# Optimization experiments

Measured on AMD Instinct MI355X. Metric: run time of the kernel, lower is better.

Reference implementation:

```python
import jax, jax.numpy as jnp
import numpy as np

R_SAFE = 0.8

def setup_inputs() -> dict:
    key = jax.random.key(0)
    ks = jax.random.split(key, 12)
    B, F, H1, H21, H22, C = 524288, 10, 128, 32, 32, 2
    def lin(k, fan_in, fan_out):
        k1, k2 = jax.random.split(k)
        bound = 1.0 / np.sqrt(fan_in)
        W = jax.random.uniform(k1, (fan_out, fan_in), jnp.float32, -bound, bound)
        b = jax.random.uniform(k2, (fan_out,), jnp.float32, -bound, bound)
        return W, b
    W1, b1 = lin(ks[0], F, H1)
    W21, b21 = lin(ks[1], H1, H21)
    W22, b22 = lin(ks[2], H1, H22)
    W31, b31 = lin(ks[3], H21, C)
    W32, b32 = lin(ks[4], H22, 1)
    obs = jax.random.normal(ks[5], (B, F), jnp.float32)
    return {"obs": obs, "W1": W1, "b1": b1, "W21": W21, "b21": b21,
            "W22": W22, "b22": b22, "W31": W31, "b31": b31, "W32": W32, "b32": b32}

def _forward(obs, W1, b1, W21, b21, W22, b22, W31, b31, W32, b32):
    x = jax.nn.silu(obs @ W1.T + b1)          # [B, H1]
    x21 = jax.nn.silu(x @ W21.T + b21)        # [B, H21]
    x22 = jax.nn.silu(x @ W22.T + b22)        # [B, H22]
    unom = x21 @ W31.T + b31                  # [B, 2]
    alpha = 4.0 * jax.nn.sigmoid((x22 @ W32.T + b32)[:, 0])  # [B]
    rel_x, rel_y = obs[:, 6], obs[:, 7]
    v_hx, v_hy = obs[:, 8], obs[:, 9]
    barrier = rel_x**2 + rel_y**2 - R_SAFE**2
    lf = -2.0 * (rel_x * v_hx + rel_y * v_hy)
    # single inequality G u <= h with G = [-2 rel_x, -2 rel_y]
    G = jnp.stack([-2.0 * rel_x, -2.0 * rel_y], axis=1)      # [B, 2]
    h = lf + alpha * barrier                                  # [B]
    # QP: min ||u - unom||^2 s.t. G u <= h  ->  halfspace projection (exact KKT)
    gg = jnp.sum(G * G, axis=1)                               # [B]
    viol = jnp.sum(G * unom, axis=1) - h                      # [B]
    lam = jnp.where(gg > 0, jax.nn.relu(viol) / jnp.maximum(gg, 1e-12), 0.0)
    return unom - lam[:, None] * G

def reference(obs, W1, b1, W21, b21, W22, b22, W31, b31, W32, b32):
    return _forward(obs, W1, b1, W21, b21, W22, b22, W31, b31, W32, b32)
```

## Files before the change

### kernel.cpp

```cpp
#include <hip/hip_runtime.h>


typedef _Float16 half8 __attribute__((ext_vector_type(8)));
typedef float floatx4 __attribute__((ext_vector_type(4)));

#define TPB 256
#define NW  4

#define WS_FRAG 0
#define WS_B2Q  26624

__device__ __forceinline__ float fast_sigmoid(float z) {
    return __builtin_amdgcn_rcpf(1.0f + __expf(-z));
}

__global__ __launch_bounds__(256) void prep_kernel(
    const float* __restrict__ W1,  const float* __restrict__ b1,
    const float* __restrict__ W21, const float* __restrict__ b21,
    const float* __restrict__ W22, const float* __restrict__ b22,
    const float* __restrict__ W31, const float* __restrict__ b31,
    const float* __restrict__ W32, const float* __restrict__ b32,
    unsigned char* __restrict__ ws)
{
    const int tid  = blockIdx.x * 256 + threadIdx.x;
    const int lane = tid & 63;
    const int m    = lane & 15;
    const int q    = lane >> 4;

    if (tid < 26 * 64) {
        const int f = tid >> 6;
        float v[8];
        if (f < 8) {
            const float* wr = W1 + (f * 16 + m) * 10;
            #pragma unroll
            for (int j = 0; j < 8; ++j) {
                const int k = q * 8 + j;
                v[j] = (k < 10) ? wr[k] : (k == 10 ? b1[f * 16 + m] : 0.0f);
            }
        } else if (f < 24) {
            const int f2 = f - 8, nt2 = f2 >> 2, kt = f2 & 3;
            const int n2 = nt2 * 16 + m;
            const float* wr = (n2 < 32) ? (W21 + n2 * 128)
                                        : (W22 + (n2 - 32) * 128);
            #pragma unroll
            for (int j = 0; j < 8; ++j) {
                const int H = (2 * kt + (j >> 2)) * 16 + q * 4 + (j & 3);
                v[j] = wr[H];
            }
        } else {
            const int kt3 = f - 24;
            #pragma unroll
            for (int j = 0; j < 8; ++j) {
                const int H3 = (2 * kt3 + (j >> 2)) * 16 + q * 4 + (j & 3);
                float x = 0.0f;
                if (m == 0)      x = (H3 < 32)  ? W31[H3]       : 0.0f;
                else if (m == 1) x = (H3 < 32)  ? W31[32 + H3]  : 0.0f;
                else if (m == 2) x = (H3 >= 32) ? W32[H3 - 32]  : 0.0f;
                v[j] = x;
            }
        }
        half8 h;
        #pragma unroll
        for (int j = 0; j < 8; ++j) h[j] = (_Float16)v[j];
        ((half8*)(ws + WS_FRAG))[tid] = h;
    }
    if (tid < 16) {
        const int nt2 = tid >> 2, qq = tid & 3;
        float4 v;
        float* vp = (float*)&v;
        #pragma unroll
        for (int r = 0; r < 4; ++r) {
            const int n2 = nt2 * 16 + qq * 4 + r;
            vp[r] = (n2 < 32) ? b21[n2] : b22[n2 - 32];
        }
        ((float4*)(ws + WS_B2Q))[tid] = v;
    }
}

__global__ __launch_bounds__(TPB, 2) void barriernet_kernel(
    const float* __restrict__ obs,
    const unsigned char* __restrict__ ws,
    const float* __restrict__ b31, const float* __restrict__ b32,
    float* __restrict__ out, int B)
{
    const int tid  = threadIdx.x;
    const int wave = tid >> 6;
    const int lane = tid & 63;
    const int m    = lane & 15;
    const int q    = lane >> 4;

    const half8* wf = (const half8*)(ws + WS_FRAG);
    half8 w1f[8], w2f[16], w3f0, w3f1;
    #pragma unroll
    for (int nt = 0; nt < 8; ++nt)  w1f[nt] = wf[nt * 64 + lane];
    #pragma unroll
    for (int f2 = 0; f2 < 16; ++f2) w2f[f2] = wf[(8 + f2) * 64 + lane];
    w3f0 = wf[24 * 64 + lane];
    w3f1 = wf[25 * 64 + lane];

    const float4* bt = (const float4*)(ws + WS_B2Q);
    float4 b2q[4];
    #pragma unroll
    for (int nt2 = 0; nt2 < 4; ++nt2) b2q[nt2] = bt[nt2 * 4 + q];

    const float bu0 = b31[0], bu1 = b31[1], bz3 = b32[0];

    const int tiles = (B + 15) >> 4;
    const int tbase = (blockIdx.x * NW + wave) * 2;

    const float* orow[2];
    half8 xf[2];
    int lrow0[2];
    #pragma unroll
    for (int p = 0; p < 2; ++p) {
        int tile = tbase + p;
        if (tile >= tiles) tile = tiles - 1;
        int lr = (tile << 4) + m;
        if (lr >= B) lr = B - 1;
        lrow0[p] = lr;
        orow[p] = obs + (size_t)lr * 10;

        float g0=0,g1=0,g2=0,g3=0,g4=0,g5=0,g6=0,g7=0;
        if (q == 0) {
            float2 p0 = *(const float2*)(orow[p] + 0);
            float2 p1 = *(const float2*)(orow[p] + 2);
            float2 p2 = *(const float2*)(orow[p] + 4);
            float2 p3 = *(const float2*)(orow[p] + 6);
            g0=p0.x; g1=p0.y; g2=p1.x; g3=p1.y;
            g4=p2.x; g5=p2.y; g6=p3.x; g7=p3.y;
        } else if (q == 1) {
            float2 pp = *(const float2*)(orow[p] + 8);
            g0=pp.x; g1=pp.y;
            g2=1.0f;
        }
        xf[p][0]=(_Float16)g0; xf[p][1]=(_Float16)g1;
        xf[p][2]=(_Float16)g2; xf[p][3]=(_Float16)g3;
        xf[p][4]=(_Float16)g4; xf[p][5]=(_Float16)g5;
        xf[p][6]=(_Float16)g6; xf[p][7]=(_Float16)g7;
    }

    floatx4 acc[2][8];
    #pragma unroll
    for (int nt = 0; nt < 8; ++nt) {
        #pragma unroll
        for (int p = 0; p < 2; ++p) {
            floatx4 z = {0.0f, 0.0f, 0.0f, 0.0f};
            acc[p][nt] = __builtin_amdgcn_mfma_f32_16x16x32_f16(
                             w1f[nt], xf[p], z, 0, 0, 0);
        }
    }

    half8 b2f[2][4];
    #pragma unroll
    for (int p = 0; p < 2; ++p) {
        #pragma unroll
        for (int kt = 0; kt < 4; ++kt) {
            half8 bf;
            #pragma unroll
            for (int jj = 0; jj < 4; ++jj) {
                float z0 = acc[p][2 * kt][jj];
                float z1 = acc[p][2 * kt + 1][jj];
                bf[jj]     = (_Float16)(z0 * fast_sigmoid(z0));
                bf[jj + 4] = (_Float16)(z1 * fast_sigmoid(z1));
            }
            b2f[p][kt] = bf;
        }
    }

    floatx4 acc2[2][4];
    #pragma unroll
    for (int nt2 = 0; nt2 < 4; ++nt2) {
        #pragma unroll
        for (int p = 0; p < 2; ++p) {
            floatx4 z = {b2q[nt2].x, b2q[nt2].y, b2q[nt2].z, b2q[nt2].w};
            #pragma unroll
            for (int kt = 0; kt < 4; ++kt)
                z = __builtin_amdgcn_mfma_f32_16x16x32_f16(
                        w2f[nt2 * 4 + kt], b2f[p][kt], z, 0, 0, 0);
            acc2[p][nt2] = z;
        }
    }

    half8 b3f[2][2];
    #pragma unroll
    for (int p = 0; p < 2; ++p) {
        #pragma unroll
        for (int kt3 = 0; kt3 < 2; ++kt3) {
            half8 bf;
            #pragma unroll
            for (int jj = 0; jj < 4; ++jj) {
                float z0 = acc2[p][2 * kt3][jj];
                float z1 = acc2[p][2 * kt3 + 1][jj];
                bf[jj]     = (_Float16)(z0 * fast_sigmoid(z0));
                bf[jj + 4] = (_Float16)(z1 * fast_sigmoid(z1));
            }
            b3f[p][kt3] = bf;
        }
    }

    #pragma unroll
    for (int p = 0; p < 2; ++p) {
        floatx4 d = {0.0f, 0.0f, 0.0f, 0.0f};
        d = __builtin_amdgcn_mfma_f32_16x16x32_f16(w3f0, b3f[p][0], d, 0, 0, 0);
        d = __builtin_amdgcn_mfma_f32_16x16x32_f16(w3f1, b3f[p][1], d, 0, 0, 0);
        if (q == 0) {
            const float u0  = d[0] + bu0;
            const float u1  = d[1] + bu1;
            const float z32 = d[2] + bz3;
            const float alpha = 4.0f * fast_sigmoid(z32);

            const float2 rxy = *(const float2*)(orow[p] + 6);
            const float2 vxy = *(const float2*)(orow[p] + 8);
            const float rx = rxy.x, ry = rxy.y, vx = vxy.x, vy = vxy.y;

            const float barrier = rx * rx + ry * ry - 0.64f;
            const float lf = -2.0f * (rx * vx + ry * vy);
            const float gx = -2.0f * rx, gy = -2.0f * ry;
            const float h  = lf + alpha * barrier;
            const float gg = gx * gx + gy * gy;
            const float viol = gx * u0 + gy * u1 - h;
            float lam = 0.0f;
            if (gg > 0.0f) lam = fmaxf(viol, 0.0f) / fmaxf(gg, 1e-12f);

            float2 r;
            r.x = fmaf(-lam, gx, u0);
            r.y = fmaf(-lam, gy, u1);
            *(float2*)(out + (size_t)lrow0[p] * 2) = r;
        }
    }
}

extern "C" void kernel_launch(void* const* d_in, const int* in_sizes, int n_in,
                              void* d_out, int out_size, void* d_ws, size_t ws_size,
                              hipStream_t stream) {
    const float* obs = (const float*)d_in[0];
    const float* W1  = (const float*)d_in[1];
    const float* b1  = (const float*)d_in[2];
    const float* W21 = (const float*)d_in[3];
    const float* b21 = (const float*)d_in[4];
    const float* W22 = (const float*)d_in[5];
    const float* b22 = (const float*)d_in[6];
    const float* W31 = (const float*)d_in[7];
    const float* b31 = (const float*)d_in[8];
    const float* W32 = (const float*)d_in[9];
    const float* b32 = (const float*)d_in[10];

    unsigned char* ws = (unsigned char*)d_ws;

    prep_kernel<<<7, 256, 0, stream>>>(W1, b1, W21, b21, W22, b22,
                                       W31, b31, W32, b32, ws);

    const int B = in_sizes[0] / 10;
    const int tiles = (B + 15) / 16;
    const int pairs = (tiles + 1) / 2;
    const int grid  = (pairs + NW - 1) / NW;

    barriernet_kernel<<<grid, TPB, 0, stream>>>(obs, ws, b31, b32,
                                                (float*)d_out, B);
}
```

Baseline: 124.0 us.

## Process four row tiles per wave and fuse layer-1 MFMA with SiLU

Each wave now handles four 16-row tiles instead of two, so the per-wave cost of loading weight fragments into registers is spread over more rows. The grid shrinks to match. Layer-1 MFMAs are also computed per k-slice and passed straight into SiLU, so the full acc[p][8] array is never held live. The cost is more registers per wave for the extra tiles, which may reduce occupancy, and fewer waves in flight for hiding latency.

```diff
diff --git a/kernel.cpp b/kernel.cpp
--- a/kernel.cpp
+++ b/kernel.cpp
@@ -6,6 +6,7 @@
 
 #define TPB 256
 #define NW  4
+#define NT  4
 
 #define WS_FRAG 0
 #define WS_B2Q  26624
@@ -106,13 +107,13 @@
     const float bu0 = b31[0], bu1 = b31[1], bz3 = b32[0];
 
     const int tiles = (B + 15) >> 4;
-    const int tbase = (blockIdx.x * NW + wave) * 2;
-
-    const float* orow[2];
-    half8 xf[2];
-    int lrow0[2];
-    #pragma unroll
-    for (int p = 0; p < 2; ++p) {
+    const int tbase = (blockIdx.x * NW + wave) * NT;
+
+    const float* orow[NT];
+    half8 xf[NT];
+    int lrow0[NT];
+    #pragma unroll
+    for (int p = 0; p < NT; ++p) {
         int tile = tbase + p;
         if (tile >= tiles) tile = tiles - 1;
         int lr = (tile << 4) + m;
@@ -139,27 +140,20 @@
         xf[p][6]=(_Float16)g6; xf[p][7]=(_Float16)g7;
     }
 
-    floatx4 acc[2][8];
-    #pragma unroll
-    for (int nt = 0; nt < 8; ++nt) {
-        #pragma unroll
-        for (int p = 0; p < 2; ++p) {
-            floatx4 z = {0.0f, 0.0f, 0.0f, 0.0f};
-            acc[p][nt] = __builtin_amdgcn_mfma_f32_16x16x32_f16(
-                             w1f[nt], xf[p], z, 0, 0, 0);
-        }
-    }
-
-    half8 b2f[2][4];
-    #pragma unroll
-    for (int p = 0; p < 2; ++p) {
-        #pragma unroll
-        for (int kt = 0; kt < 4; ++kt) {
+    half8 b2f[NT][4];
+    #pragma unroll
+    for (int kt = 0; kt < 4; ++kt) {
+        #pragma unroll
+        for (int p = 0; p < NT; ++p) {
+            const floatx4 zz = {0.0f, 0.0f, 0.0f, 0.0f};
+            floatx4 a0 = __builtin_amdgcn_mfma_f32_16x16x32_f16(
+                             w1f[2 * kt],     xf[p], zz, 0, 0, 0);
+            floatx4 a1 = __builtin_amdgcn_mfma_f32_16x16x32_f16(
+                             w1f[2 * kt + 1], xf[p], zz, 0, 0, 0);
             half8 bf;
             #pragma unroll
             for (int jj = 0; jj < 4; ++jj) {
-                float z0 = acc[p][2 * kt][jj];
-                float z1 = acc[p][2 * kt + 1][jj];
+                float z0 = a0[jj], z1 = a1[jj];
                 bf[jj]     = (_Float16)(z0 * fast_sigmoid(z0));
                 bf[jj + 4] = (_Float16)(z1 * fast_sigmoid(z1));
             }
@@ -167,11 +161,11 @@
         }
     }
 
-    floatx4 acc2[2][4];
+    floatx4 acc2[NT][4];
     #pragma unroll
     for (int nt2 = 0; nt2 < 4; ++nt2) {
         #pragma unroll
-        for (int p = 0; p < 2; ++p) {
+        for (int p = 0; p < NT; ++p) {
             floatx4 z = {b2q[nt2].x, b2q[nt2].y, b2q[nt2].z, b2q[nt2].w};
             #pragma unroll
             for (int kt = 0; kt < 4; ++kt)
@@ -181,11 +175,11 @@
         }
     }
 
-    half8 b3f[2][2];
-    #pragma unroll
-    for (int p = 0; p < 2; ++p) {
-        #pragma unroll
-        for (int kt3 = 0; kt3 < 2; ++kt3) {
+    half8 b3f[NT][2];
+    #pragma unroll
+    for (int kt3 = 0; kt3 < 2; ++kt3) {
+        #pragma unroll
+        for (int p = 0; p < NT; ++p) {
             half8 bf;
             #pragma unroll
             for (int jj = 0; jj < 4; ++jj) {
@@ -199,7 +193,7 @@
     }
 
     #pragma unroll
-    for (int p = 0; p < 2; ++p) {
+    for (int p = 0; p < NT; ++p) {
         floatx4 d = {0.0f, 0.0f, 0.0f, 0.0f};
         d = __builtin_amdgcn_mfma_f32_16x16x32_f16(w3f0, b3f[p][0], d, 0, 0, 0);
         d = __builtin_amdgcn_mfma_f32_16x16x32_f16(w3f1, b3f[p][1], d, 0, 0, 0);
@@ -252,8 +246,8 @@
 
     const int B = in_sizes[0] / 10;
     const int tiles = (B + 15) / 16;
-    const int pairs = (tiles + 1) / 2;
-    const int grid  = (pairs + NW - 1) / NW;
+    const int wavesN = (tiles + NT - 1) / NT;
+    const int grid  = (wavesN + NW - 1) / NW;
 
     barriernet_kernel<<<grid, TPB, 0, stream>>>(obs, ws, b31, b32,
                                                 (float*)d_out, B);
```

Measured after the change: 120.4 us. 2.9% less time.

## Stage layer-2 weights in LDS, share reciprocal in SiLU pairs, raise occupancy

Applied to the files above, without the earlier changes.

Layer-2 weight fragments move from per-thread registers into shared memory, loaded once per block. MFMA fragments are read from LDS per use, which cuts VGPR pressure so launch bounds can allow 3 blocks per CU instead of 2. SiLU is computed in pairs with one reciprocal shared across two values, and the exponent is clamped to avoid overflow. Layer-1 MFMAs are interleaved with their activations, and the QP division becomes an approximate reciprocal. In exchange it adds a block barrier and LDS reads on the critical path, and the approximate reciprocals lower precision slightly.

```diff
diff --git a/kernel.cpp b/kernel.cpp
--- a/kernel.cpp
+++ b/kernel.cpp
@@ -8,10 +8,21 @@
 #define NW  4
 
 #define WS_FRAG 0
+#define WS_W2   8192
 #define WS_B2Q  26624
 
 __device__ __forceinline__ float fast_sigmoid(float z) {
     return __builtin_amdgcn_rcpf(1.0f + __expf(-z));
+}
+
+__device__ __forceinline__ void silu_pair(float z0, float z1,
+                                          _Float16* o0, _Float16* o1) {
+    float e0 = __expf(fminf(-z0, 30.0f));
+    float e1 = __expf(fminf(-z1, 30.0f));
+    float d0 = 1.0f + e0, d1 = 1.0f + e1;
+    float r  = __builtin_amdgcn_rcpf(d0 * d1);
+    *o0 = (_Float16)(z0 * d1 * r);
+    *o1 = (_Float16)(z1 * d0 * r);
 }
 
 __global__ __launch_bounds__(256) void prep_kernel(
@@ -77,24 +88,32 @@
     }
 }
 
-__global__ __launch_bounds__(TPB, 2) void barriernet_kernel(
+__global__ __launch_bounds__(TPB, 3) void barriernet_kernel(
     const float* __restrict__ obs,
     const unsigned char* __restrict__ ws,
     const float* __restrict__ b31, const float* __restrict__ b32,
     float* __restrict__ out, int B)
 {
+    __shared__ __align__(16) unsigned char lds[16384];
+
     const int tid  = threadIdx.x;
     const int wave = tid >> 6;
     const int lane = tid & 63;
     const int m    = lane & 15;
     const int q    = lane >> 4;
 
+    {
+        const float4* src = (const float4*)(ws + WS_W2);
+        float4* dst = (float4*)lds;
+        #pragma unroll
+        for (int i = 0; i < 4; ++i) dst[tid + 256 * i] = src[tid + 256 * i];
+    }
+    __syncthreads();
+
     const half8* wf = (const half8*)(ws + WS_FRAG);
-    half8 w1f[8], w2f[16], w3f0, w3f1;
-    #pragma unroll
-    for (int nt = 0; nt < 8; ++nt)  w1f[nt] = wf[nt * 64 + lane];
-    #pragma unroll
-    for (int f2 = 0; f2 < 16; ++f2) w2f[f2] = wf[(8 + f2) * 64 + lane];
+    half8 w1f[8], w3f0, w3f1;
+    #pragma unroll
+    for (int nt = 0; nt < 8; ++nt) w1f[nt] = wf[nt * 64 + lane];
     w3f0 = wf[24 * 64 + lane];
     w3f1 = wf[25 * 64 + lane];
 
@@ -104,6 +123,8 @@
     for (int nt2 = 0; nt2 < 4; ++nt2) b2q[nt2] = bt[nt2 * 4 + q];
 
     const float bu0 = b31[0], bu1 = b31[1], bz3 = b32[0];
+
+    const half8* w2l = ((const half8*)lds) + lane;
 
     const int tiles = (B + 15) >> 4;
     const int tbase = (blockIdx.x * NW + wave) * 2;
@@ -139,60 +160,55 @@
         xf[p][6]=(_Float16)g6; xf[p][7]=(_Float16)g7;
     }
 
-    floatx4 acc[2][8];
-    #pragma unroll
-    for (int nt = 0; nt < 8; ++nt) {
+    half8 b2f[2][4];
+    #pragma unroll
+    for (int kt = 0; kt < 4; ++kt) {
         #pragma unroll
         for (int p = 0; p < 2; ++p) {
-            floatx4 z = {0.0f, 0.0f, 0.0f, 0.0f};
-            acc[p][nt] = __builtin_amdgcn_mfma_f32_16x16x32_f16(
-                             w1f[nt], xf[p], z, 0, 0, 0);
-        }
-    }
-
-    half8 b2f[2][4];
-    #pragma unroll
-    for (int p = 0; p < 2; ++p) {
+            const floatx4 zz = {0.0f, 0.0f, 0.0f, 0.0f};
+            floatx4 a0 = __builtin_amdgcn_mfma_f32_16x16x32_f16(
+                             w1f[2 * kt],     xf[p], zz, 0, 0, 0);
+            floatx4 a1 = __builtin_amdgcn_mfma_f32_16x16x32_f16(
+                             w1f[2 * kt + 1], xf[p], zz, 0, 0, 0);
+            half8 bf;
+            #pragma unroll
+            for (int jj = 0; jj < 4; ++jj) {
+                _Float16 o0, o1;
+                silu_pair(a0[jj], a1[jj], &o0, &o1);
+                bf[jj] = o0; bf[jj + 4] = o1;
+            }
+            b2f[p][kt] = bf;
+        }
+    }
+
+    floatx4 acc2[2][4];
+    #pragma unroll
+    for (int nt2 = 0; nt2 < 4; ++nt2) {
+        floatx4 zi = {b2q[nt2].x, b2q[nt2].y, b2q[nt2].z, b2q[nt2].w};
+        acc2[0][nt2] = zi;
+        acc2[1][nt2] = zi;
         #pragma unroll
         for (int kt = 0; kt < 4; ++kt) {
+            half8 wfr = w2l[(nt2 * 4 + kt) * 64];
+            acc2[0][nt2] = __builtin_amdgcn_mfma_f32_16x16x32_f16(
+                               wfr, b2f[0][kt], acc2[0][nt2], 0, 0, 0);
+            acc2[1][nt2] = __builtin_amdgcn_mfma_f32_16x16x32_f16(
+                               wfr, b2f[1][kt], acc2[1][nt2], 0, 0, 0);
+        }
+    }
+
+    half8 b3f[2][2];
+    #pragma unroll
+    for (int kt3 = 0; kt3 < 2; ++kt3) {
+        #pragma unroll
+        for (int p = 0; p < 2; ++p) {
             half8 bf;
             #pragma unroll
             for (int jj = 0; jj < 4; ++jj) {
-                float z0 = acc[p][2 * kt][jj];
-                float z1 = acc[p][2 * kt + 1][jj];
-                bf[jj]     = (_Float16)(z0 * fast_sigmoid(z0));
-                bf[jj + 4] = (_Float16)(z1 * fast_sigmoid(z1));
-            }
-            b2f[p][kt] = bf;
-        }
-    }
-
-    floatx4 acc2[2][4];
-    #pragma unroll
-    for (int nt2 = 0; nt2 < 4; ++nt2) {
-        #pragma unroll
-        for (int p = 0; p < 2; ++p) {
-            floatx4 z = {b2q[nt2].x, b2q[nt2].y, b2q[nt2].z, b2q[nt2].w};
-            #pragma unroll
-            for (int kt = 0; kt < 4; ++kt)
-                z = __builtin_amdgcn_mfma_f32_16x16x32_f16(
-                        w2f[nt2 * 4 + kt], b2f[p][kt], z, 0, 0, 0);
-            acc2[p][nt2] = z;
-        }
-    }
-
-    half8 b3f[2][2];
-    #pragma unroll
-    for (int p = 0; p < 2; ++p) {
-        #pragma unroll
-        for (int kt3 = 0; kt3 < 2; ++kt3) {
-            half8 bf;
-            #pragma unroll
-            for (int jj = 0; jj < 4; ++jj) {
-                float z0 = acc2[p][2 * kt3][jj];
-                float z1 = acc2[p][2 * kt3 + 1][jj];
-                bf[jj]     = (_Float16)(z0 * fast_sigmoid(z0));
-                bf[jj + 4] = (_Float16)(z1 * fast_sigmoid(z1));
+                _Float16 o0, o1;
+                silu_pair(acc2[p][2 * kt3][jj], acc2[p][2 * kt3 + 1][jj],
+                          &o0, &o1);
+                bf[jj] = o0; bf[jj + 4] = o1;
             }
             b3f[p][kt3] = bf;
         }
@@ -220,7 +236,9 @@
             const float gg = gx * gx + gy * gy;
             const float viol = gx * u0 + gy * u1 - h;
             float lam = 0.0f;
-            if (gg > 0.0f) lam = fmaxf(viol, 0.0f) / fmaxf(gg, 1e-12f);
+            if (gg > 0.0f)
+                lam = fmaxf(viol, 0.0f) *
+                      __builtin_amdgcn_rcpf(fmaxf(gg, 1e-12f));
 
             float2 r;
             r.x = fmaf(-lam, gx, u0);
```

After: 118.4 us. 4.5% less time.
